# Performance work log

Hardware: AMD Instinct MI355X
Metric: run time of the kernel (lower is better)

## Reference

```python
import jax, jax.numpy as jnp
import numpy as np

TEACHER_DIM = 512
STUDENT_DIM = 64
CHUNK_SIZE = TEACHER_DIM // STUDENT_DIM  # 8
NUM_CHUNKS = TEACHER_DIM // CHUNK_SIZE   # 64
B, H, W = 8, 96, 96


def setup_inputs() -> dict:
    key = jax.random.key(0)
    ks = jax.random.split(key, 7)
    x = jax.random.normal(ks[0], (B, TEACHER_DIM, H, W), dtype=jnp.float32)
    # stacked 1x1-conv weights: [num_chunks, out_ch, in_ch] and biases [num_chunks, out_ch]
    Wq = jax.random.normal(ks[1], (NUM_CHUNKS, CHUNK_SIZE, CHUNK_SIZE), dtype=jnp.float32)
    bq = jax.random.normal(ks[2], (NUM_CHUNKS, CHUNK_SIZE), dtype=jnp.float32)
    Wk = jax.random.normal(ks[3], (NUM_CHUNKS, CHUNK_SIZE, CHUNK_SIZE), dtype=jnp.float32)
    bk = jax.random.normal(ks[4], (NUM_CHUNKS, CHUNK_SIZE), dtype=jnp.float32)
    Wv = jax.random.normal(ks[5], (NUM_CHUNKS, CHUNK_SIZE, CHUNK_SIZE), dtype=jnp.float32)
    bv = jax.random.normal(ks[6], (NUM_CHUNKS, CHUNK_SIZE), dtype=jnp.float32)
    return {"x": x, "Wq": Wq, "bq": bq, "Wk": Wk, "bk": bk, "Wv": Wv, "bv": bv}


def reference(x, Wq, bq, Wk, bk, Wv, bv):
    b, c, h, w = x.shape
    hw = h * w
    # split channels into chunks -> [B, num_chunks, chunk_size, H*W]
    xc = x.reshape(b, NUM_CHUNKS, CHUNK_SIZE, hw)
    # 1x1 conv == per-chunk channel matmul; o=out_ch, c=in_ch, p=pixels
    q = jnp.einsum('bncp,noc->bnop', xc, Wq) + bq[None, :, :, None]
    k = jnp.einsum('bncp,noc->bnop', xc, Wk) + bk[None, :, :, None]
    v = jnp.einsum('bncp,noc->bnop', xc, Wv) + bv[None, :, :, None]
    # channel-attention: scores [B, num_chunks, chunk_size, chunk_size]
    scale = 1.0 / jnp.sqrt(jnp.asarray(hw, dtype=x.dtype))
    attn = jax.nn.softmax(jnp.einsum('bnqp,bnkp->bnqk', q, k) * scale, axis=-1)
    attended = jnp.einsum('bnqk,bnkp->bnqp', attn, v)  # [B,N,C,HW]
    # pooled = sum over chunk_size of elementwise product -> [B, num_chunks, H, W]
    pooled = jnp.sum(xc * attended, axis=2).reshape(b, NUM_CHUNKS, h, w)
    return pooled
```

## Files before the change

kernel.cpp:

```cpp
#include <hip/hip_runtime.h>

#define CHUNK 8
#define NCHUNK 64
#define TDIM 512
#define HW 9216
#define NT 768
#define NWAVE (NT/64)
#define F4_PER_CH (HW/4)
#define ITERS (F4_PER_CH/NT)

typedef float floatx4 __attribute__((ext_vector_type(4)));

__host__ __device__ constexpr int TRI(int c, int j) {
    return (c*(15-c))/2 + j;
}
__host__ __device__ constexpr int PairIdx(int c, int j) {
    return 7*c - (c*(c-1))/2 + (j - c - 1);
}

__device__ __forceinline__ unsigned bf16_rne(float f) {
    unsigned u = __float_as_uint(f);
    return (u + 0x7fffu + ((u >> 16) & 1u)) >> 16;
}
__device__ __forceinline__ float bf16_to_f(unsigned h16) {
    return __uint_as_float(h16 << 16);
}

__global__ __launch_bounds__(NT)
void lcsap_kernel(const float* __restrict__ x,
                  const float* __restrict__ Wq, const float* __restrict__ bq,
                  const float* __restrict__ Wk, const float* __restrict__ bk,
                  const float* __restrict__ Wv, const float* __restrict__ bv,
                  float* __restrict__ out)
{
    const int bid = blockIdx.x;
    const int b   = bid >> 6;
    const int n   = bid & 63;
    const int tid = threadIdx.x;
    const int lane = tid & 63;
    const int wid  = tid >> 6;

    const float* xb = x + ((size_t)(b*TDIM + n*CHUNK)) * HW;
    float* ob = out + ((size_t)(b*NCHUNK + n)) * HW;

    __shared__ uint2 xs[8][F4_PER_CH];
    __shared__ float red[NWAVE][44];
    __shared__ float Gf[64];
    __shared__ float sf[8];
    __shared__ float Mld[64];
    __shared__ float tld[8];

    float g[36], sr[8];
    #pragma unroll
    for (int i = 0; i < 36; ++i) g[i] = 0.f;
    #pragma unroll
    for (int c = 0; c < 8; ++c) sr[c] = 0.f;

    floatx4 cur[8], nxt[8];
    #pragma unroll
    for (int c = 0; c < 8; ++c)
        cur[c] = reinterpret_cast<const floatx4*>(xb + (size_t)c*HW)[tid];

    #pragma unroll
    for (int it = 0; it < ITERS; ++it) {
        const int f = tid + it*NT;
        if (it + 1 < ITERS) {
            const int fn = f + NT;
            #pragma unroll
            for (int c = 0; c < 8; ++c)
                nxt[c] = reinterpret_cast<const floatx4*>(xb + (size_t)c*HW)[fn];
        }
        #pragma unroll
        for (int c = 0; c < 8; ++c) {
            uint2 p;
            p.x = bf16_rne(cur[c][0]) | (bf16_rne(cur[c][1]) << 16);
            p.y = bf16_rne(cur[c][2]) | (bf16_rne(cur[c][3]) << 16);
            xs[c][f] = p;
        }
        #pragma unroll
        for (int u = 0; u < 4; ++u) {
            float xv[8];
            #pragma unroll
            for (int c = 0; c < 8; ++c) xv[c] = cur[c][u];
            #pragma unroll
            for (int c = 0; c < 8; ++c) sr[c] += xv[c];
            #pragma unroll
            for (int c = 0; c < 8; ++c) {
                #pragma unroll
                for (int j = c; j < 8; ++j)
                    g[TRI(c,j)] += xv[c]*xv[j];
            }
        }
        #pragma unroll
        for (int c = 0; c < 8; ++c) cur[c] = nxt[c];
    }

    #pragma unroll
    for (int i = 0; i < 36; ++i) {
        g[i] += __shfl_xor(g[i], 1);  g[i] += __shfl_xor(g[i], 2);
        g[i] += __shfl_xor(g[i], 4);  g[i] += __shfl_xor(g[i], 8);
        g[i] += __shfl_xor(g[i], 16); g[i] += __shfl_xor(g[i], 32);
    }
    #pragma unroll
    for (int c = 0; c < 8; ++c) {
        sr[c] += __shfl_xor(sr[c], 1);  sr[c] += __shfl_xor(sr[c], 2);
        sr[c] += __shfl_xor(sr[c], 4);  sr[c] += __shfl_xor(sr[c], 8);
        sr[c] += __shfl_xor(sr[c], 16); sr[c] += __shfl_xor(sr[c], 32);
    }
    if (lane == 0) {
        #pragma unroll
        for (int i = 0; i < 36; ++i) red[wid][i] = g[i];
        #pragma unroll
        for (int c = 0; c < 8; ++c) red[wid][36+c] = sr[c];
    }
    __syncthreads();
    if (tid < 44) {
        float v = 0.f;
        #pragma unroll
        for (int w = 0; w < NWAVE; ++w) v += red[w][tid];
        if (tid < 36) {
            int c = 0, base = 0;
            for (; c < 8; ++c) { int w = 8 - c; if (tid < base + w) break; base += w; }
            int j = c + (tid - base);
            Gf[c*8+j] = v;
            Gf[j*8+c] = v;
        } else {
            sf[tid-36] = v;
        }
    }
    __syncthreads();

    if (tid < 64) {
        const int qi = tid >> 3;
        const int ki = tid & 7;
        float wq[8], wk[8];
        #pragma unroll
        for (int c = 0; c < 8; ++c) {
            wq[c] = Wq[n*64 + qi*8 + c];
            wk[c] = Wk[n*64 + ki*8 + c];
        }
        float sc = 0.f, qs = 0.f, ks_ = 0.f;
        #pragma unroll
        for (int c = 0; c < 8; ++c) {
            float tmp = 0.f;
            #pragma unroll
            for (int d = 0; d < 8; ++d) tmp += Gf[c*8+d]*wk[d];
            sc += wq[c]*tmp;
            qs += wq[c]*sf[c];
            ks_ += wk[c]*sf[c];
        }
        const float bqv = bq[n*8+qi];
        const float bkv = bk[n*8+ki];
        sc += qs*bkv + bqv*ks_ + (float)HW * bqv * bkv;
        sc *= (1.0f/96.0f);

        float m = sc;
        m = fmaxf(m, __shfl_xor(m, 1, 8));
        m = fmaxf(m, __shfl_xor(m, 2, 8));
        m = fmaxf(m, __shfl_xor(m, 4, 8));
        float e = expf(sc - m);
        float se = e;
        se += __shfl_xor(se, 1, 8);
        se += __shfl_xor(se, 2, 8);
        se += __shfl_xor(se, 4, 8);
        const float attn = e / se;

        float mv = 0.f;
        #pragma unroll
        for (int k = 0; k < 8; ++k) {
            float ak = __shfl(attn, k, 8);
            mv += ak * Wv[n*64 + k*8 + ki];
        }
        Mld[qi*8 + ki] = mv;

        float tv = attn * bv[n*8 + ki];
        tv += __shfl_xor(tv, 1, 8);
        tv += __shfl_xor(tv, 2, 8);
        tv += __shfl_xor(tv, 4, 8);
        if (ki == 0) tld[qi] = tv;
    }
    __syncthreads();

    float diag[8], tt[8], su[28];
    #pragma unroll
    for (int c = 0; c < 8; ++c) { diag[c] = Mld[c*9]; tt[c] = tld[c]; }
    #pragma unroll
    for (int c = 0; c < 8; ++c) {
        #pragma unroll
        for (int j = c+1; j < 8; ++j)
            su[PairIdx(c,j)] = Mld[c*8+j] + Mld[j*8+c];
    }

    #pragma unroll
    for (int it = 0; it < ITERS; ++it) {
        const int f = tid + it*NT;
        uint2 v[8];
        #pragma unroll
        for (int c = 0; c < 8; ++c) v[c] = xs[c][f];
        floatx4 o;
        #pragma unroll
        for (int u = 0; u < 4; ++u) {
            float xv[8];
            #pragma unroll
            for (int c = 0; c < 8; ++c) {
                unsigned w32 = (u < 2) ? v[c].x : v[c].y;
                unsigned h   = (u & 1) ? (w32 >> 16) : (w32 & 0xffffu);
                xv[c] = bf16_to_f(h);
            }
            float acc = 0.f;
            #pragma unroll
            for (int c = 0; c < 8; ++c) acc += tt[c]*xv[c];
            #pragma unroll
            for (int c = 0; c < 8; ++c) acc += diag[c]*xv[c]*xv[c];
            #pragma unroll
            for (int c = 0; c < 8; ++c) {
                #pragma unroll
                for (int j = c+1; j < 8; ++j)
                    acc += su[PairIdx(c,j)]*xv[c]*xv[j];
            }
            o[u] = acc;
        }
        reinterpret_cast<floatx4*>(ob)[f] = o;
    }
}

extern "C" void kernel_launch(void* const* d_in, const int* in_sizes, int n_in,
                              void* d_out, int out_size, void* d_ws, size_t ws_size,
                              hipStream_t stream) {
    const float* x  = (const float*)d_in[0];
    const float* Wq = (const float*)d_in[1];
    const float* bq = (const float*)d_in[2];
    const float* Wk = (const float*)d_in[3];
    const float* bk = (const float*)d_in[4];
    const float* Wv = (const float*)d_in[5];
    const float* bv = (const float*)d_in[6];
    float* out = (float*)d_out;

    lcsap_kernel<<<dim3(512), dim3(NT), 0, stream>>>(x, Wq, bq, Wk, bk, Wv, bv, out);
}
```

Measured before the change: 54.89 us.

## Split Gram computation: stream loads with sums, off-diagonal products from LDS bf16

The load phase now walks x as a flat sequence of float4 slots, four per thread per step with double buffering. It keeps only per-channel sums and sums of squares while packing bf16 into shared memory. The 28 off-diagonal Gram products are then computed in a second pass that reads the bf16 copy from LDS. The aim is to shorten the memory-bound load loop and cut register pressure, so more loads stay in flight. The cost is an extra LDS read pass and off-diagonal Gram terms built from bf16-rounded values instead of fp32, which lowers precision.

```diff
diff --git a/kernel.cpp b/kernel.cpp
--- a/kernel.cpp
+++ b/kernel.cpp
@@ -5,15 +5,14 @@
 #define TDIM 512
 #define HW 9216
 #define NT 768
-#define NWAVE (NT/64)
-#define F4_PER_CH (HW/4)
-#define ITERS (F4_PER_CH/NT)
+#define NWAVE 12
+#define F4C 2304
+#define NSLOT (8*F4C)
+#define CITERS (NSLOT/NT)
+#define GITERS (F4C/NT)
 
 typedef float floatx4 __attribute__((ext_vector_type(4)));
 
-__host__ __device__ constexpr int TRI(int c, int j) {
-    return (c*(15-c))/2 + j;
-}
 __host__ __device__ constexpr int PairIdx(int c, int j) {
     return 7*c - (c*(c-1))/2 + (j - c - 1);
 }
@@ -21,9 +20,6 @@
 __device__ __forceinline__ unsigned bf16_rne(float f) {
     unsigned u = __float_as_uint(f);
     return (u + 0x7fffu + ((u >> 16) & 1u)) >> 16;
-}
-__device__ __forceinline__ float bf16_to_f(unsigned h16) {
-    return __uint_as_float(h16 << 16);
 }
 
 __global__ __launch_bounds__(NT)
@@ -42,88 +38,112 @@
 
     const float* xb = x + ((size_t)(b*TDIM + n*CHUNK)) * HW;
     float* ob = out + ((size_t)(b*NCHUNK + n)) * HW;
-
-    __shared__ uint2 xs[8][F4_PER_CH];
+    const floatx4* xf4 = reinterpret_cast<const floatx4*>(xb);
+
+    __shared__ uint2 xs[NSLOT];
     __shared__ float red[NWAVE][44];
     __shared__ float Gf[64];
     __shared__ float sf[8];
     __shared__ float Mld[64];
     __shared__ float tld[8];
 
-    float g[36], sr[8];
-    #pragma unroll
-    for (int i = 0; i < 36; ++i) g[i] = 0.f;
-    #pragma unroll
-    for (int c = 0; c < 8; ++c) sr[c] = 0.f;
-
-    floatx4 cur[8], nxt[8];
-    #pragma unroll
-    for (int c = 0; c < 8; ++c)
-        cur[c] = reinterpret_cast<const floatx4*>(xb + (size_t)c*HW)[tid];
-
-    #pragma unroll
-    for (int it = 0; it < ITERS; ++it) {
-        const int f = tid + it*NT;
-        if (it + 1 < ITERS) {
-            const int fn = f + NT;
-            #pragma unroll
-            for (int c = 0; c < 8; ++c)
-                nxt[c] = reinterpret_cast<const floatx4*>(xb + (size_t)c*HW)[fn];
-        }
-        #pragma unroll
-        for (int c = 0; c < 8; ++c) {
+    float accs[8], accd[8];
+    #pragma unroll
+    for (int c = 0; c < 8; ++c) { accs[c] = 0.f; accd[c] = 0.f; }
+
+    floatx4 buf[2][4];
+    #pragma unroll
+    for (int k = 0; k < 4; ++k)
+        buf[0][k] = xf4[k*NT + tid];
+
+    #pragma unroll
+    for (int obt = 0; obt < 6; ++obt) {
+        const int pb = obt & 1, nb = pb ^ 1;
+        if (obt < 5) {
+            #pragma unroll
+            for (int k = 0; k < 4; ++k)
+                buf[nb][k] = xf4[(obt*4 + 4 + k)*NT + tid];
+        }
+        #pragma unroll
+        for (int k = 0; k < 4; ++k) {
+            const int it = obt*4 + k;
+            const int c  = it / 3;
+            const int s  = it*NT + tid;
+            floatx4 v = buf[pb][k];
+            #pragma unroll
+            for (int u = 0; u < 4; ++u) {
+                accs[c] += v[u];
+                accd[c] += v[u]*v[u];
+            }
             uint2 p;
-            p.x = bf16_rne(cur[c][0]) | (bf16_rne(cur[c][1]) << 16);
-            p.y = bf16_rne(cur[c][2]) | (bf16_rne(cur[c][3]) << 16);
-            xs[c][f] = p;
+            p.x = bf16_rne(v[0]) | (bf16_rne(v[1]) << 16);
+            p.y = bf16_rne(v[2]) | (bf16_rne(v[3]) << 16);
+            xs[s] = p;
+        }
+    }
+    __syncthreads();
+
+    float g[28];
+    #pragma unroll
+    for (int i = 0; i < 28; ++i) g[i] = 0.f;
+
+    #pragma unroll
+    for (int it = 0; it < GITERS; ++it) {
+        const int f = it*NT + tid;
+        float xv[8][4];
+        #pragma unroll
+        for (int c = 0; c < 8; ++c) {
+            uint2 w = xs[c*F4C + f];
+            xv[c][0] = __uint_as_float(w.x << 16);
+            xv[c][1] = __uint_as_float(w.x & 0xffff0000u);
+            xv[c][2] = __uint_as_float(w.y << 16);
+            xv[c][3] = __uint_as_float(w.y & 0xffff0000u);
         }
         #pragma unroll
         for (int u = 0; u < 4; ++u) {
-            float xv[8];
-            #pragma unroll
-            for (int c = 0; c < 8; ++c) xv[c] = cur[c][u];
-            #pragma unroll
-            for (int c = 0; c < 8; ++c) sr[c] += xv[c];
             #pragma unroll
             for (int c = 0; c < 8; ++c) {
                 #pragma unroll
-                for (int j = c; j < 8; ++j)
-                    g[TRI(c,j)] += xv[c]*xv[j];
+                for (int j = c+1; j < 8; ++j)
+                    g[PairIdx(c,j)] += xv[c][u]*xv[j][u];
             }
         }
-        #pragma unroll
-        for (int c = 0; c < 8; ++c) cur[c] = nxt[c];
-    }
-
-    #pragma unroll
-    for (int i = 0; i < 36; ++i) {
+    }
+
+    #pragma unroll
+    for (int i = 0; i < 28; ++i) {
         g[i] += __shfl_xor(g[i], 1);  g[i] += __shfl_xor(g[i], 2);
         g[i] += __shfl_xor(g[i], 4);  g[i] += __shfl_xor(g[i], 8);
         g[i] += __shfl_xor(g[i], 16); g[i] += __shfl_xor(g[i], 32);
     }
     #pragma unroll
     for (int c = 0; c < 8; ++c) {
-        sr[c] += __shfl_xor(sr[c], 1);  sr[c] += __shfl_xor(sr[c], 2);
-        sr[c] += __shfl_xor(sr[c], 4);  sr[c] += __shfl_xor(sr[c], 8);
-        sr[c] += __shfl_xor(sr[c], 16); sr[c] += __shfl_xor(sr[c], 32);
+        accd[c] += __shfl_xor(accd[c], 1);  accd[c] += __shfl_xor(accd[c], 2);
+        accd[c] += __shfl_xor(accd[c], 4);  accd[c] += __shfl_xor(accd[c], 8);
+        accd[c] += __shfl_xor(accd[c], 16); accd[c] += __shfl_xor(accd[c], 32);
+        accs[c] += __shfl_xor(accs[c], 1);  accs[c] += __shfl_xor(accs[c], 2);
+        accs[c] += __shfl_xor(accs[c], 4);  accs[c] += __shfl_xor(accs[c], 8);
+        accs[c] += __shfl_xor(accs[c], 16); accs[c] += __shfl_xor(accs[c], 32);
     }
     if (lane == 0) {
         #pragma unroll
-        for (int i = 0; i < 36; ++i) red[wid][i] = g[i];
-        #pragma unroll
-        for (int c = 0; c < 8; ++c) red[wid][36+c] = sr[c];
+        for (int i = 0; i < 28; ++i) red[wid][i] = g[i];
+        #pragma unroll
+        for (int c = 0; c < 8; ++c) { red[wid][28+c] = accd[c]; red[wid][36+c] = accs[c]; }
     }
     __syncthreads();
     if (tid < 44) {
         float v = 0.f;
         #pragma unroll
         for (int w = 0; w < NWAVE; ++w) v += red[w][tid];
-        if (tid < 36) {
+        if (tid < 28) {
             int c = 0, base = 0;
-            for (; c < 8; ++c) { int w = 8 - c; if (tid < base + w) break; base += w; }
-            int j = c + (tid - base);
+            for (; c < 8; ++c) { int w = 7 - c; if (tid < base + w) break; base += w; }
+            int j = c + 1 + (tid - base);
             Gf[c*8+j] = v;
             Gf[j*8+c] = v;
+        } else if (tid < 36) {
+            Gf[(tid-28)*9] = v;
         } else {
             sf[tid-36] = v;
         }
@@ -192,31 +212,30 @@
     }
 
     #pragma unroll
-    for (int it = 0; it < ITERS; ++it) {
-        const int f = tid + it*NT;
-        uint2 v[8];
-        #pragma unroll
-        for (int c = 0; c < 8; ++c) v[c] = xs[c][f];
+    for (int it = 0; it < GITERS; ++it) {
+        const int f = it*NT + tid;
+        float xv[8][4];
+        #pragma unroll
+        for (int c = 0; c < 8; ++c) {
+            uint2 w = xs[c*F4C + f];
+            xv[c][0] = __uint_as_float(w.x << 16);
+            xv[c][1] = __uint_as_float(w.x & 0xffff0000u);
+            xv[c][2] = __uint_as_float(w.y << 16);
+            xv[c][3] = __uint_as_float(w.y & 0xffff0000u);
+        }
         floatx4 o;
         #pragma unroll
         for (int u = 0; u < 4; ++u) {
-            float xv[8];
-            #pragma unroll
-            for (int c = 0; c < 8; ++c) {
-                unsigned w32 = (u < 2) ? v[c].x : v[c].y;
-                unsigned h   = (u & 1) ? (w32 >> 16) : (w32 & 0xffffu);
-                xv[c] = bf16_to_f(h);
-            }
             float acc = 0.f;
             #pragma unroll
-            for (int c = 0; c < 8; ++c) acc += tt[c]*xv[c];
-            #pragma unroll
-            for (int c = 0; c < 8; ++c) acc += diag[c]*xv[c]*xv[c];
+            for (int c = 0; c < 8; ++c) acc += tt[c]*xv[c][u];
+            #pragma unroll
+            for (int c = 0; c < 8; ++c) acc += diag[c]*xv[c][u]*xv[c][u];
             #pragma unroll
             for (int c = 0; c < 8; ++c) {
                 #pragma unroll
                 for (int j = c+1; j < 8; ++j)
-                    acc += su[PairIdx(c,j)]*xv[c]*xv[j];
+                    acc += su[PairIdx(c,j)]*xv[c][u]*xv[j][u];
             }
             o[u] = acc;
         }
```

New measurement: 60.91 us. 1.11x slower.
